# Kernel tuning notes

Hardware: AMD Instinct MI355X
Metric: run time of the kernel (lower is better)

The kernel has to match this reference:

```python
import jax, jax.numpy as jnp
import numpy as np

B, OBJ, INP, HID = 8, 128, 64, 256
D = 3 * INP  # concatenated per-object feature dim


def setup_inputs() -> dict:
    key = jax.random.key(0)
    ks = jax.random.split(key, 12)
    s = 0.02
    return {
        "x0": jax.random.normal(ks[0], (B, OBJ, INP), jnp.float32),
        "x1": jax.random.normal(ks[1], (B, OBJ, INP), jnp.float32),
        "x2": jax.random.normal(ks[2], (B, OBJ, INP), jnp.float32),
        # weights stored [in, out] so forward is x @ w + b
        "w_enc": jax.random.normal(ks[3], (2 * D, HID), jnp.float32) * s,
        "b_enc": jnp.zeros((HID,), jnp.float32),
        "w1": jax.random.normal(ks[4], (HID, HID), jnp.float32) * s,
        "b1": jnp.zeros((HID,), jnp.float32),
        "w2": jax.random.normal(ks[5], (HID, HID), jnp.float32) * s,
        "b2": jnp.zeros((HID,), jnp.float32),
        "w3": jax.random.normal(ks[6], (HID, HID), jnp.float32) * s,
        "b3": jnp.zeros((HID,), jnp.float32),
        "wd1": jax.random.normal(ks[7], (HID, HID), jnp.float32) * s,
        "bd1": jnp.zeros((HID,), jnp.float32),
        "wd2": jax.random.normal(ks[8], (HID, INP), jnp.float32) * s,
        "bd2": jnp.zeros((INP,), jnp.float32),
    }


def reference(x0, x1, x2, w_enc, b_enc, w1, b1, w2, b2, w3, b3, wd1, bd1, wd2, bd2):
    x = jnp.concatenate([x0, x1, x2], axis=-1)  # [B, N, D]
    # Fused equivalent of Linear(cat(e1, e2)): split w_enc rows into the part
    # acting on the first-object features and the second-object features, then
    # broadcast-add instead of materializing the [B,N,N,2D] concat tensor.
    ea = jnp.einsum("bnd,dh->bnh", x, w_enc[:D])   # acts on data_e1
    eb = jnp.einsum("bnd,dh->bnh", x, w_enc[D:])   # acts on data_e2
    h = jax.nn.relu(ea[:, :, None, :] + eb[:, None, :, :] + b_enc)  # [B,N,N,H]
    h = jax.nn.relu(h @ w1 + b1)
    h = jax.nn.relu(h @ w2 + b2)
    h = h @ w3 + b3              # fc3 has no activation before the mean
    pooled = h.mean(axis=2)      # [B, N, H]
    out = jax.nn.relu(pooled @ wd1 + bd1) @ wd2 + bd2  # [B, N, INP]
    return out
```

## Files before the change

### kernel.cpp

```cpp
#include <hip/hip_runtime.h>
#include <stdint.h>


#define HID 256
#define NOBJ 128
#define NROW 1024

typedef __attribute__((ext_vector_type(8))) short short8;
typedef __attribute__((ext_vector_type(4))) float float4v;
typedef __attribute__((ext_vector_type(16))) float float16v;
typedef __attribute__((ext_vector_type(2))) unsigned int uint2v;

__device__ __forceinline__ unsigned int f2bf_u(float f) {
    unsigned int u = __builtin_bit_cast(unsigned int, f);
    u += 0x7fffu + ((u >> 16) & 1u);
    return u >> 16;
}
__device__ __forceinline__ unsigned int pack2(float a, float b) {
    return f2bf_u(a) | (f2bf_u(b) << 16);
}
__device__ __forceinline__ float relu(float v) { return v > 0.f ? v : 0.f; }

__device__ __forceinline__ void lds_barrier() {
    asm volatile("s_waitcnt lgkmcnt(0)\n\ts_barrier" ::: "memory");
}

__global__ void setup_kernel(const float* __restrict__ x0, const float* __restrict__ x1,
                             const float* __restrict__ x2, const float* __restrict__ w_enc,
                             const float* __restrict__ b_enc,
                             const float* __restrict__ w1, const float* __restrict__ w2,
                             const float* __restrict__ w3, const float* __restrict__ b3,
                             const float* __restrict__ wd1, const float* __restrict__ bd1,
                             unsigned short* __restrict__ wt,
                             float* __restrict__ ea, float* __restrict__ eb,
                             float* __restrict__ W34, float* __restrict__ b34) {
    const int bx = blockIdx.x, t = threadIdx.x;
    __shared__ float lw[256][33];
    __shared__ float xs[2][192];
    if (bx < 16) {
        const int m = bx >> 3, tau = bx & 7;
        const float* w = (m == 0) ? w1 : w2;
        const int n = t & 31, kk = t >> 5;
#pragma unroll
        for (int rep = 0; rep < 32; ++rep) {
            int k = rep * 8 + kk;
            lw[k][n] = w[k * 256 + tau * 32 + n];
        }
        __syncthreads();
        unsigned short* outp = wt + (m * 8 + tau) * 8192;
        const int lane = t & 63, wq = t >> 6;
        const int h5 = lane >> 5, l31n = lane & 31;
#pragma unroll
        for (int rep = 0; rep < 4; ++rep) {
            const int kb = wq * 4 + rep;
            short8 v;
#pragma unroll
            for (int e = 0; e < 8; ++e)
                v[e] = (short)f2bf_u(lw[kb * 16 + h5 * 8 + e][l31n]);
            *(short8*)(outp + kb * 512 + lane * 8) = v;
        }
        return;
    }
    if (bx < 528) {
        const int e = bx - 16;
        for (int idx = t; idx < 384; idx += 256) {
            int r = idx / 192, d = idx % 192;
            int row = e * 2 + r;
            float v = (d < 64) ? x0[row * 64 + d]
                    : (d < 128) ? x1[row * 64 + d - 64]
                    : x2[row * 64 + d - 128];
            xs[r][d] = v;
        }
        __syncthreads();
        float aA[2] = {0.f, 0.f}, aB[2] = {0.f, 0.f};
#pragma unroll 16
        for (int d = 0; d < 192; ++d) {
            float wa = w_enc[d * 256 + t];
            float wb = w_enc[(192 + d) * 256 + t];
#pragma unroll
            for (int r = 0; r < 2; ++r) { aA[r] += xs[r][d] * wa; aB[r] += xs[r][d] * wb; }
        }
        float be = b_enc[t];
#pragma unroll
        for (int r = 0; r < 2; ++r) {
            ea[(e * 2 + r) * 256 + t] = aA[r] + be;
            eb[(e * 2 + r) * 256 + t] = aB[r];
        }
        return;
    }
    if (bx < 784) {
        const int m = bx - 528;
        float a = 0.f;
#pragma unroll 8
        for (int k = 0; k < 256; ++k) a += w3[m * 256 + k] * wd1[k * 256 + t];
        W34[m * 256 + t] = a;
        return;
    }
    {
        float a = bd1[t];
#pragma unroll 8
        for (int k = 0; k < 256; ++k) a += b3[k] * wd1[k * 256 + t];
        b34[t] = a;
    }
}

__global__ __launch_bounds__(256, 2) void pair_kernel(
        const float* __restrict__ ea, const float* __restrict__ eb,
        const unsigned short* __restrict__ wt,
        const float* __restrict__ b1, const float* __restrict__ b2,
        const float* __restrict__ W34, const float* __restrict__ b34,
        const float* __restrict__ wd2, const float* __restrict__ bd2,
        float* __restrict__ out) {
    __shared__ __align__(16) unsigned short hbuf[128 * 256];

    const int w = blockIdx.x, b = w >> 7;
    const int t = threadIdx.x, wv = t >> 6, lane = t & 63;
    const int l31 = lane & 31, h5 = lane >> 5;
    const int n0 = wv * 64;

    const unsigned short* aptr = wt + lane * 8;

    short8 af[4][2], bfr[2][4];
#pragma unroll
    for (int pg = 0; pg < 3; ++pg) {
        af[pg][0] = *(const short8*)(aptr + ((wv * 2 + 0) * 16 + pg) * 512);
        af[pg][1] = *(const short8*)(aptr + ((wv * 2 + 1) * 16 + pg) * 512);
    }

    {
        const float4v va = *(const float4v*)(ea + w * 256 + lane * 4);
        const float* ebbase = eb + (b * NOBJ) * 256;
        const int c = lane >> 1, sub = (lane & 1) * 4;
#pragma unroll 4
        for (int jj = 0; jj < 32; ++jj) {
            const int j = wv * 32 + jj;
            float4v vb = *(const float4v*)(ebbase + j * 256 + lane * 4);
            int addr = j * 256 + ((c ^ (j & 31)) << 3) + sub;
            *(uint2v*)(hbuf + addr) = (uint2v){
                pack2(relu(va[0] + vb[0]), relu(va[1] + vb[1])),
                pack2(relu(va[2] + vb[2]), relu(va[3] + vb[3]))};
        }
    }
    lds_barrier();

    int jb[4];
#pragma unroll
    for (int tj = 0; tj < 4; ++tj) jb[tj] = (tj * 32 + l31) * 256;
#pragma unroll
    for (int tj = 0; tj < 4; ++tj)
        bfr[0][tj] = *(const short8*)(hbuf + jb[tj] + ((h5 ^ l31) << 3));

    float16v acc[2][4];

#pragma unroll
    for (int l = 0; l < 2; ++l) {
        const float* bias = (l == 0) ? b1 : b2;
#pragma unroll
        for (int tn = 0; tn < 2; ++tn)
#pragma unroll
            for (int q = 0; q < 4; ++q) {
                float4v bv = *(const float4v*)(bias + n0 + tn * 32 + q * 8 + h5 * 4);
#pragma unroll
                for (int i = 0; i < 4; ++i)
#pragma unroll
                    for (int tj = 0; tj < 4; ++tj)
                        acc[tn][tj][q * 4 + i] = bv[i];
            }
#pragma unroll
        for (int kb = 0; kb < 16; ++kb) {
            const int g = l * 16 + kb, gp = g + 3;
            if (gp < 32) {
                const int lp = gp >> 4, kp = gp & 15;
                af[gp & 3][0] = *(const short8*)(aptr + ((lp * 8 + wv * 2 + 0) * 16 + kp) * 512);
                af[gp & 3][1] = *(const short8*)(aptr + ((lp * 8 + wv * 2 + 1) * 16 + kp) * 512);
            }
            if (kb < 15) {
                const int off = ((((kb + 1) * 2 + h5) ^ l31) << 3);
#pragma unroll
                for (int tj = 0; tj < 4; ++tj)
                    bfr[(kb + 1) & 1][tj] = *(const short8*)(hbuf + jb[tj] + off);
            }
#pragma unroll
            for (int tn = 0; tn < 2; ++tn)
#pragma unroll
                for (int tj = 0; tj < 4; ++tj)
                    acc[tn][tj] = __builtin_amdgcn_mfma_f32_32x32x16_bf16(
                        af[g & 3][tn], bfr[kb & 1][tj], acc[tn][tj], 0, 0, 0);
        }
        lds_barrier();

        if (l == 0) {
#pragma unroll
            for (int tn = 0; tn < 2; ++tn)
#pragma unroll
                for (int q = 0; q < 4; ++q) {
                    const int nb_ = n0 + tn * 32 + 8 * q + 4 * h5;
                    const int cn = nb_ >> 3, sub = nb_ & 7;
#pragma unroll
                    for (int tj = 0; tj < 4; ++tj) {
                        const int j = tj * 32 + l31;
                        int addr = j * 256 + ((cn ^ l31) << 3) + sub;
                        *(uint2v*)(hbuf + addr) = (uint2v){
                            pack2(relu(acc[tn][tj][q * 4]), relu(acc[tn][tj][q * 4 + 1])),
                            pack2(relu(acc[tn][tj][q * 4 + 2]), relu(acc[tn][tj][q * 4 + 3]))};
                    }
                }
            lds_barrier();
#pragma unroll
            for (int tj = 0; tj < 4; ++tj)
                bfr[0][tj] = *(const short8*)(hbuf + jb[tj] + ((h5 ^ l31) << 3));
        }
    }

    float* fs = (float*)hbuf;
    {
#pragma unroll
        for (int tn = 0; tn < 2; ++tn)
#pragma unroll
            for (int r = 0; r < 16; ++r) {
                float s = relu(acc[tn][0][r]) + relu(acc[tn][1][r])
                        + relu(acc[tn][2][r]) + relu(acc[tn][3][r]);
                s += __shfl_xor(s, 1);
                s += __shfl_xor(s, 2);
                s += __shfl_xor(s, 4);
                s += __shfl_xor(s, 8);
                s += __shfl_xor(s, 16);
                if (l31 == 0) {
                    const int n = n0 + tn * 32 + (r & 3) + 8 * (r >> 2) + 4 * h5;
                    fs[n] = s * 0.0078125f;
                }
            }
    }
    __syncthreads();
    {
        float p0 = 0.f, p1 = 0.f, p2 = 0.f, p3 = 0.f;
        const float* wp = W34 + (wv * 64) * 256 + lane;
#pragma unroll 8
        for (int kk = 0; kk < 64; ++kk) {
            float mv = fs[wv * 64 + kk];
            p0 += mv * wp[kk * 256];
            p1 += mv * wp[kk * 256 + 64];
            p2 += mv * wp[kk * 256 + 128];
            p3 += mv * wp[kk * 256 + 192];
        }
        fs[256 + wv * 256 + lane]       = p0;
        fs[256 + wv * 256 + 64 + lane]  = p1;
        fs[256 + wv * 256 + 128 + lane] = p2;
        fs[256 + wv * 256 + 192 + lane] = p3;
    }
    __syncthreads();
    fs[1280 + t] = relu(fs[256 + t] + fs[512 + t] + fs[768 + t] + fs[1024 + t] + b34[t]);
    __syncthreads();
    {
        float p = 0.f;
        const float* w2p = wd2 + (wv * 64) * 64 + lane;
#pragma unroll 8
        for (int kk = 0; kk < 64; ++kk) p += fs[1280 + wv * 64 + kk] * w2p[kk * 64];
        fs[1536 + wv * 64 + lane] = p;
    }
    __syncthreads();
    if (t < 64)
        out[w * 64 + t] = fs[1536 + t] + fs[1600 + t] + fs[1664 + t] + fs[1728 + t] + bd2[t];
}

extern "C" void kernel_launch(void* const* d_in, const int* in_sizes, int n_in,
                              void* d_out, int out_size, void* d_ws, size_t ws_size,
                              hipStream_t stream) {
    const float* x0    = (const float*)d_in[0];
    const float* x1    = (const float*)d_in[1];
    const float* x2    = (const float*)d_in[2];
    const float* w_enc = (const float*)d_in[3];
    const float* b_enc = (const float*)d_in[4];
    const float* w1    = (const float*)d_in[5];
    const float* b1    = (const float*)d_in[6];
    const float* w2    = (const float*)d_in[7];
    const float* b2    = (const float*)d_in[8];
    const float* w3    = (const float*)d_in[9];
    const float* b3    = (const float*)d_in[10];
    const float* wd1   = (const float*)d_in[11];
    const float* bd1   = (const float*)d_in[12];
    const float* wd2   = (const float*)d_in[13];
    const float* bd2   = (const float*)d_in[14];
    float* out = (float*)d_out;

    unsigned short* wt = (unsigned short*)d_ws;
    float* ea  = (float*)((char*)d_ws + 3 * 65536 * sizeof(unsigned short));
    float* eb  = ea + NROW * HID;
    float* W34 = eb + NROW * HID;
    float* b34 = W34 + 256 * 256;

    setup_kernel<<<785, 256, 0, stream>>>(x0, x1, x2, w_enc, b_enc, w1, w2,
                                          w3, b3, wd1, bd1, wt, ea, eb, W34, b34);
    pair_kernel<<<NROW, 256, 0, stream>>>(ea, eb, wt, b1, b2, W34, b34, wd2, bd2, out);
}
```

Before: 155.1 us.

## Split pair tile into two 64-row passes to halve LDS and raise occupancy

Each pair block now processes its 128 partner objects in two passes of 64, which halves the bf16 LDS activation buffer (64 KB to 32 KB) and the accumulator register count. Partial pooled sums are carried between passes in a small shared array, and launch bounds are raised from 2 to 4 blocks per CU. The aim is more resident waves to hide latency, at the cost of reloading the weight fragments twice per block and a shallower weight prefetch (depth 1 instead of 3).

```diff
diff --git a/kernel.cpp b/kernel.cpp
--- a/kernel.cpp
+++ b/kernel.cpp
@@ -104,14 +104,15 @@
     }
 }
 
-__global__ __launch_bounds__(256, 2) void pair_kernel(
+__global__ __launch_bounds__(256, 4) void pair_kernel(
         const float* __restrict__ ea, const float* __restrict__ eb,
         const unsigned short* __restrict__ wt,
         const float* __restrict__ b1, const float* __restrict__ b2,
         const float* __restrict__ W34, const float* __restrict__ b34,
         const float* __restrict__ wd2, const float* __restrict__ bd2,
         float* __restrict__ out) {
-    __shared__ __align__(16) unsigned short hbuf[128 * 256];
+    __shared__ __align__(16) unsigned short hbuf[64 * 256];
+    __shared__ float ms[HID];
 
     const int w = blockIdx.x, b = w >> 7;
     const int t = threadIdx.x, wv = t >> 6, lane = t & 63;
@@ -120,106 +121,104 @@
 
     const unsigned short* aptr = wt + lane * 8;
 
-    short8 af[4][2], bfr[2][4];
-#pragma unroll
-    for (int pg = 0; pg < 3; ++pg) {
-        af[pg][0] = *(const short8*)(aptr + ((wv * 2 + 0) * 16 + pg) * 512);
-        af[pg][1] = *(const short8*)(aptr + ((wv * 2 + 1) * 16 + pg) * 512);
-    }
-
-    {
-        const float4v va = *(const float4v*)(ea + w * 256 + lane * 4);
-        const float* ebbase = eb + (b * NOBJ) * 256;
-        const int c = lane >> 1, sub = (lane & 1) * 4;
+    short8 af[2][2], bfr[2][2];
+    float16v acc[2][2];
+
+#pragma unroll 1
+    for (int pass = 0; pass < 2; ++pass) {
+#pragma unroll
+        for (int tn = 0; tn < 2; ++tn)
+            af[0][tn] = *(const short8*)(aptr + ((wv * 2 + tn) * 16) * 512);
+
+        {
+            const float4v va = *(const float4v*)(ea + w * 256 + lane * 4);
+            const float* ebbase = eb + (b * NOBJ + pass * 64) * 256;
+            const int c = lane >> 1, sub = (lane & 1) * 4;
 #pragma unroll 4
-        for (int jj = 0; jj < 32; ++jj) {
-            const int j = wv * 32 + jj;
-            float4v vb = *(const float4v*)(ebbase + j * 256 + lane * 4);
-            int addr = j * 256 + ((c ^ (j & 31)) << 3) + sub;
-            *(uint2v*)(hbuf + addr) = (uint2v){
-                pack2(relu(va[0] + vb[0]), relu(va[1] + vb[1])),
-                pack2(relu(va[2] + vb[2]), relu(va[3] + vb[3]))};
-        }
-    }
-    lds_barrier();
-
-    int jb[4];
-#pragma unroll
-    for (int tj = 0; tj < 4; ++tj) jb[tj] = (tj * 32 + l31) * 256;
-#pragma unroll
-    for (int tj = 0; tj < 4; ++tj)
-        bfr[0][tj] = *(const short8*)(hbuf + jb[tj] + ((h5 ^ l31) << 3));
-
-    float16v acc[2][4];
-
-#pragma unroll
-    for (int l = 0; l < 2; ++l) {
-        const float* bias = (l == 0) ? b1 : b2;
+            for (int jj = 0; jj < 16; ++jj) {
+                const int j = wv * 16 + jj;
+                float4v vb = *(const float4v*)(ebbase + j * 256 + lane * 4);
+                int addr = j * 256 + ((c ^ (j & 31)) << 3) + sub;
+                *(uint2v*)(hbuf + addr) = (uint2v){
+                    pack2(relu(va[0] + vb[0]), relu(va[1] + vb[1])),
+                    pack2(relu(va[2] + vb[2]), relu(va[3] + vb[3]))};
+            }
+        }
+        lds_barrier();
+
+        int jb[2];
+#pragma unroll
+        for (int tj = 0; tj < 2; ++tj) jb[tj] = (tj * 32 + l31) * 256;
+#pragma unroll
+        for (int tj = 0; tj < 2; ++tj)
+            bfr[0][tj] = *(const short8*)(hbuf + jb[tj] + ((h5 ^ l31) << 3));
+
+#pragma unroll
+        for (int l = 0; l < 2; ++l) {
+            const float* bias = (l == 0) ? b1 : b2;
+#pragma unroll
+            for (int tn = 0; tn < 2; ++tn)
+#pragma unroll
+                for (int q = 0; q < 4; ++q) {
+                    float4v bv = *(const float4v*)(bias + n0 + tn * 32 + q * 8 + h5 * 4);
+#pragma unroll
+                    for (int i = 0; i < 4; ++i)
+#pragma unroll
+                        for (int tj = 0; tj < 2; ++tj)
+                            acc[tn][tj][q * 4 + i] = bv[i];
+                }
+#pragma unroll
+            for (int kb = 0; kb < 16; ++kb) {
+                const int g = l * 16 + kb, gp = g + 1;
+                if (gp < 32) {
+                    const int lp = gp >> 4, kp = gp & 15;
+#pragma unroll
+                    for (int tn = 0; tn < 2; ++tn)
+                        af[gp & 1][tn] = *(const short8*)(aptr + ((lp * 8 + wv * 2 + tn) * 16 + kp) * 512);
+                }
+                if (kb < 15) {
+                    const int off = ((((kb + 1) * 2 + h5) ^ l31) << 3);
+#pragma unroll
+                    for (int tj = 0; tj < 2; ++tj)
+                        bfr[(kb + 1) & 1][tj] = *(const short8*)(hbuf + jb[tj] + off);
+                }
+#pragma unroll
+                for (int tn = 0; tn < 2; ++tn)
+#pragma unroll
+                    for (int tj = 0; tj < 2; ++tj)
+                        acc[tn][tj] = __builtin_amdgcn_mfma_f32_32x32x16_bf16(
+                            af[g & 1][tn], bfr[kb & 1][tj], acc[tn][tj], 0, 0, 0);
+            }
+            lds_barrier();
+
+            if (l == 0) {
+#pragma unroll
+                for (int tn = 0; tn < 2; ++tn)
+#pragma unroll
+                    for (int q = 0; q < 4; ++q) {
+                        const int nb_ = n0 + tn * 32 + 8 * q + 4 * h5;
+                        const int cn = nb_ >> 3, sub = nb_ & 7;
+#pragma unroll
+                        for (int tj = 0; tj < 2; ++tj) {
+                            const int j = tj * 32 + l31;
+                            int addr = j * 256 + ((cn ^ l31) << 3) + sub;
+                            *(uint2v*)(hbuf + addr) = (uint2v){
+                                pack2(relu(acc[tn][tj][q * 4]), relu(acc[tn][tj][q * 4 + 1])),
+                                pack2(relu(acc[tn][tj][q * 4 + 2]), relu(acc[tn][tj][q * 4 + 3]))};
+                        }
+                    }
+                lds_barrier();
+#pragma unroll
+                for (int tj = 0; tj < 2; ++tj)
+                    bfr[0][tj] = *(const short8*)(hbuf + jb[tj] + ((h5 ^ l31) << 3));
+            }
+        }
+
 #pragma unroll
         for (int tn = 0; tn < 2; ++tn)
 #pragma unroll
-            for (int q = 0; q < 4; ++q) {
-                float4v bv = *(const float4v*)(bias + n0 + tn * 32 + q * 8 + h5 * 4);
-#pragma unroll
-                for (int i = 0; i < 4; ++i)
-#pragma unroll
-                    for (int tj = 0; tj < 4; ++tj)
-                        acc[tn][tj][q * 4 + i] = bv[i];
-            }
-#pragma unroll
-        for (int kb = 0; kb < 16; ++kb) {
-            const int g = l * 16 + kb, gp = g + 3;
-            if (gp < 32) {
-                const int lp = gp >> 4, kp = gp & 15;
-                af[gp & 3][0] = *(const short8*)(aptr + ((lp * 8 + wv * 2 + 0) * 16 + kp) * 512);
-                af[gp & 3][1] = *(const short8*)(aptr + ((lp * 8 + wv * 2 + 1) * 16 + kp) * 512);
-            }
-            if (kb < 15) {
-                const int off = ((((kb + 1) * 2 + h5) ^ l31) << 3);
-#pragma unroll
-                for (int tj = 0; tj < 4; ++tj)
-                    bfr[(kb + 1) & 1][tj] = *(const short8*)(hbuf + jb[tj] + off);
-            }
-#pragma unroll
-            for (int tn = 0; tn < 2; ++tn)
-#pragma unroll
-                for (int tj = 0; tj < 4; ++tj)
-                    acc[tn][tj] = __builtin_amdgcn_mfma_f32_32x32x16_bf16(
-                        af[g & 3][tn], bfr[kb & 1][tj], acc[tn][tj], 0, 0, 0);
-        }
-        lds_barrier();
-
-        if (l == 0) {
-#pragma unroll
-            for (int tn = 0; tn < 2; ++tn)
-#pragma unroll
-                for (int q = 0; q < 4; ++q) {
-                    const int nb_ = n0 + tn * 32 + 8 * q + 4 * h5;
-                    const int cn = nb_ >> 3, sub = nb_ & 7;
-#pragma unroll
-                    for (int tj = 0; tj < 4; ++tj) {
-                        const int j = tj * 32 + l31;
-                        int addr = j * 256 + ((cn ^ l31) << 3) + sub;
-                        *(uint2v*)(hbuf + addr) = (uint2v){
-                            pack2(relu(acc[tn][tj][q * 4]), relu(acc[tn][tj][q * 4 + 1])),
-                            pack2(relu(acc[tn][tj][q * 4 + 2]), relu(acc[tn][tj][q * 4 + 3]))};
-                    }
-                }
-            lds_barrier();
-#pragma unroll
-            for (int tj = 0; tj < 4; ++tj)
-                bfr[0][tj] = *(const short8*)(hbuf + jb[tj] + ((h5 ^ l31) << 3));
-        }
-    }
-
-    float* fs = (float*)hbuf;
-    {
-#pragma unroll
-        for (int tn = 0; tn < 2; ++tn)
-#pragma unroll
             for (int r = 0; r < 16; ++r) {
-                float s = relu(acc[tn][0][r]) + relu(acc[tn][1][r])
-                        + relu(acc[tn][2][r]) + relu(acc[tn][3][r]);
+                float s = relu(acc[tn][0][r]) + relu(acc[tn][1][r]);
                 s += __shfl_xor(s, 1);
                 s += __shfl_xor(s, 2);
                 s += __shfl_xor(s, 4);
@@ -227,40 +226,43 @@
                 s += __shfl_xor(s, 16);
                 if (l31 == 0) {
                     const int n = n0 + tn * 32 + (r & 3) + 8 * (r >> 2) + 4 * h5;
-                    fs[n] = s * 0.0078125f;
-                }
-            }
-    }
-    __syncthreads();
+                    if (pass == 0) ms[n] = s;
+                    else           ms[n] = (ms[n] + s) * 0.0078125f;
+                }
+            }
+    }
+    __syncthreads();
+
+    float* fs = (float*)hbuf;
     {
         float p0 = 0.f, p1 = 0.f, p2 = 0.f, p3 = 0.f;
         const float* wp = W34 + (wv * 64) * 256 + lane;
 #pragma unroll 8
         for (int kk = 0; kk < 64; ++kk) {
-            float mv = fs[wv * 64 + kk];
+            float mv = ms[wv * 64 + kk];
             p0 += mv * wp[kk * 256];
             p1 += mv * wp[kk * 256 + 64];
             p2 += mv * wp[kk * 256 + 128];
             p3 += mv * wp[kk * 256 + 192];
         }
-        fs[256 + wv * 256 + lane]       = p0;
-        fs[256 + wv * 256 + 64 + lane]  = p1;
-        fs[256 + wv * 256 + 128 + lane] = p2;
-        fs[256 + wv * 256 + 192 + lane] = p3;
-    }
-    __syncthreads();
-    fs[1280 + t] = relu(fs[256 + t] + fs[512 + t] + fs[768 + t] + fs[1024 + t] + b34[t]);
+        fs[wv * 256 + lane]       = p0;
+        fs[wv * 256 + 64 + lane]  = p1;
+        fs[wv * 256 + 128 + lane] = p2;
+        fs[wv * 256 + 192 + lane] = p3;
+    }
+    __syncthreads();
+    fs[1024 + t] = relu(fs[t] + fs[256 + t] + fs[512 + t] + fs[768 + t] + b34[t]);
     __syncthreads();
     {
         float p = 0.f;
         const float* w2p = wd2 + (wv * 64) * 64 + lane;
 #pragma unroll 8
-        for (int kk = 0; kk < 64; ++kk) p += fs[1280 + wv * 64 + kk] * w2p[kk * 64];
-        fs[1536 + wv * 64 + lane] = p;
+        for (int kk = 0; kk < 64; ++kk) p += fs[1024 + wv * 64 + kk] * w2p[kk * 64];
+        fs[1280 + wv * 64 + lane] = p;
     }
     __syncthreads();
     if (t < 64)
-        out[w * 64 + t] = fs[1536 + t] + fs[1600 + t] + fs[1664 + t] + fs[1728 + t] + bd2[t];
+        out[w * 64 + t] = fs[1280 + t] + fs[1344 + t] + fs[1408 + t] + fs[1472 + t] + bd2[t];
 }
 
 extern "C" void kernel_launch(void* const* d_in, const int* in_sizes, int n_in,
```

New measurement: 208.1 us. 1.34x slower.

## Split decoder MLP out of pair kernel into batched decoder kernel

Applied to the files above, without the earlier changes.

Moves the per-row decoder GEMV (W34 then wd2) out of the pair kernel tail into a separate kernel. The pair kernel now writes only the pooled message vector, and the decoder kernel handles 8 rows per block so each W34/wd2 element is loaded once and reused across 8 rows instead of once per row. It also moves the LDS barrier after the MFMA loop inside the layer-boundary branch, removing it from the other iterations. The cost is an extra kernel launch and a global round-trip for the message buffer.

```diff
diff --git a/kernel.cpp b/kernel.cpp
--- a/kernel.cpp
+++ b/kernel.cpp
@@ -108,10 +108,9 @@
         const float* __restrict__ ea, const float* __restrict__ eb,
         const unsigned short* __restrict__ wt,
         const float* __restrict__ b1, const float* __restrict__ b2,
-        const float* __restrict__ W34, const float* __restrict__ b34,
-        const float* __restrict__ wd2, const float* __restrict__ bd2,
-        float* __restrict__ out) {
+        float* __restrict__ msg) {
     __shared__ __align__(16) unsigned short hbuf[128 * 256];
+    __shared__ float ms[HID];
 
     const int w = blockIdx.x, b = w >> 7;
     const int t = threadIdx.x, wv = t >> 6, lane = t & 63;
@@ -187,9 +186,9 @@
                     acc[tn][tj] = __builtin_amdgcn_mfma_f32_32x32x16_bf16(
                         af[g & 3][tn], bfr[kb & 1][tj], acc[tn][tj], 0, 0, 0);
         }
-        lds_barrier();
 
         if (l == 0) {
+            lds_barrier();
 #pragma unroll
             for (int tn = 0; tn < 2; ++tn)
 #pragma unroll
@@ -212,55 +211,68 @@
         }
     }
 
-    float* fs = (float*)hbuf;
-    {
-#pragma unroll
-        for (int tn = 0; tn < 2; ++tn)
-#pragma unroll
-            for (int r = 0; r < 16; ++r) {
-                float s = relu(acc[tn][0][r]) + relu(acc[tn][1][r])
-                        + relu(acc[tn][2][r]) + relu(acc[tn][3][r]);
-                s += __shfl_xor(s, 1);
-                s += __shfl_xor(s, 2);
-                s += __shfl_xor(s, 4);
-                s += __shfl_xor(s, 8);
-                s += __shfl_xor(s, 16);
-                if (l31 == 0) {
-                    const int n = n0 + tn * 32 + (r & 3) + 8 * (r >> 2) + 4 * h5;
-                    fs[n] = s * 0.0078125f;
-                }
+#pragma unroll
+    for (int tn = 0; tn < 2; ++tn)
+#pragma unroll
+        for (int r = 0; r < 16; ++r) {
+            float s = relu(acc[tn][0][r]) + relu(acc[tn][1][r])
+                    + relu(acc[tn][2][r]) + relu(acc[tn][3][r]);
+            s += __shfl_xor(s, 1);
+            s += __shfl_xor(s, 2);
+            s += __shfl_xor(s, 4);
+            s += __shfl_xor(s, 8);
+            s += __shfl_xor(s, 16);
+            if (l31 == 0) {
+                const int n = n0 + tn * 32 + (r & 3) + 8 * (r >> 2) + 4 * h5;
+                ms[n] = s * 0.0078125f;
             }
-    }
-    __syncthreads();
-    {
-        float p0 = 0.f, p1 = 0.f, p2 = 0.f, p3 = 0.f;
-        const float* wp = W34 + (wv * 64) * 256 + lane;
-#pragma unroll 8
-        for (int kk = 0; kk < 64; ++kk) {
-            float mv = fs[wv * 64 + kk];
-            p0 += mv * wp[kk * 256];
-            p1 += mv * wp[kk * 256 + 64];
-            p2 += mv * wp[kk * 256 + 128];
-            p3 += mv * wp[kk * 256 + 192];
-        }
-        fs[256 + wv * 256 + lane]       = p0;
-        fs[256 + wv * 256 + 64 + lane]  = p1;
-        fs[256 + wv * 256 + 128 + lane] = p2;
-        fs[256 + wv * 256 + 192 + lane] = p3;
-    }
-    __syncthreads();
-    fs[1280 + t] = relu(fs[256 + t] + fs[512 + t] + fs[768 + t] + fs[1024 + t] + b34[t]);
-    __syncthreads();
-    {
-        float p = 0.f;
-        const float* w2p = wd2 + (wv * 64) * 64 + lane;
-#pragma unroll 8
-        for (int kk = 0; kk < 64; ++kk) p += fs[1280 + wv * 64 + kk] * w2p[kk * 64];
-        fs[1536 + wv * 64 + lane] = p;
-    }
+        }
     __syncthreads();
     if (t < 64)
-        out[w * 64 + t] = fs[1536 + t] + fs[1600 + t] + fs[1664 + t] + fs[1728 + t] + bd2[t];
+        *(float4v*)(msg + w * 256 + t * 4) = *(const float4v*)(ms + t * 4);
+}
+
+__global__ __launch_bounds__(256) void decoder_kernel(
+        const float* __restrict__ msg, const float* __restrict__ W34,
+        const float* __restrict__ b34, const float* __restrict__ wd2,
+        const float* __restrict__ bd2, float* __restrict__ out) {
+    __shared__ float ml[8][256];
+    __shared__ float tl[8][256];
+    const int bx = blockIdx.x, t = threadIdx.x;
+    const int r0 = bx * 8;
+
+#pragma unroll
+    for (int r = 0; r < 8; ++r) ml[r][t] = msg[(r0 + r) * 256 + t];
+    __syncthreads();
+
+    {
+        float a[8];
+        const float bb = b34[t];
+#pragma unroll
+        for (int r = 0; r < 8; ++r) a[r] = bb;
+#pragma unroll 8
+        for (int k = 0; k < 256; ++k) {
+            const float wv_ = W34[k * 256 + t];
+#pragma unroll
+            for (int r = 0; r < 8; ++r) a[r] += ml[r][k] * wv_;
+        }
+#pragma unroll
+        for (int r = 0; r < 8; ++r) tl[r][t] = relu(a[r]);
+    }
+    __syncthreads();
+
+    {
+        const int o = t & 63, rg = t >> 6;
+        float a0 = bd2[o], a1 = a0;
+#pragma unroll 8
+        for (int k = 0; k < 256; ++k) {
+            const float wv_ = wd2[k * 64 + o];
+            a0 += tl[2 * rg][k] * wv_;
+            a1 += tl[2 * rg + 1][k] * wv_;
+        }
+        out[(r0 + 2 * rg) * 64 + o]     = a0;
+        out[(r0 + 2 * rg + 1) * 64 + o] = a1;
+    }
 }
 
 extern "C" void kernel_launch(void* const* d_in, const int* in_sizes, int n_in,
@@ -288,8 +300,10 @@
     float* eb  = ea + NROW * HID;
     float* W34 = eb + NROW * HID;
     float* b34 = W34 + 256 * 256;
+    float* msg = b34 + 256;
 
     setup_kernel<<<785, 256, 0, stream>>>(x0, x1, x2, w_enc, b_enc, w1, w2,
                                           w3, b3, wd1, bd1, wt, ea, eb, W34, b34);
-    pair_kernel<<<NROW, 256, 0, stream>>>(ea, eb, wt, b1, b2, W34, b34, wd2, bd2, out);
-}
+    pair_kernel<<<NROW, 256, 0, stream>>>(ea, eb, wt, b1, b2, msg);
+    decoder_kernel<<<NROW / 8, 256, 0, stream>>>(msg, W34, b34, wd2, bd2, out);
+}
```

Result: slower. 167.1 us (+7.8%).
